# Performance work log

Measured on AMD Instinct MI355X. Metric: run time of the kernel, lower is better.

The kernel has to match this reference:

```python
import jax, jax.numpy as jnp
import numpy as np

N = 50000      # nodes
E = 800000     # edges (before self-loops)
D_IN = 64
D_OUT = 64


def setup_inputs() -> dict:
    key = jax.random.key(0)
    k1, k2, k3 = jax.random.split(key, 3)
    x = jax.random.normal(k1, (N, D_IN), dtype=jnp.float32)
    edge_index = jax.random.randint(k2, (2, E), 0, N, dtype=jnp.int64)
    # Glorot-ish init for the GCN linear weight
    W = jax.random.normal(k3, (D_IN, D_OUT), dtype=jnp.float32) * (1.0 / np.sqrt(D_IN))
    b = jnp.zeros((D_OUT,), dtype=jnp.float32)
    return {"x": x, "edge_index": edge_index, "W": W, "b": b}


def reference(x, edge_index, W, b):
    # GCNConv: add self-loops, symmetric normalization D^-1/2 (A+I) D^-1/2,
    # linear transform, scatter-add aggregation, bias; then ReLU.
    # Dropout is treated in eval mode (identity) for determinism.
    n = x.shape[0]
    loop = jnp.arange(n, dtype=edge_index.dtype)
    src = jnp.concatenate([edge_index[0], loop])  # [E+N]
    dst = jnp.concatenate([edge_index[1], loop])  # [E+N]

    ones = jnp.ones(src.shape[0], dtype=x.dtype)
    deg = jax.ops.segment_sum(ones, dst, num_segments=n)            # [N]
    dis = jnp.where(deg > 0, jax.lax.rsqrt(deg), 0.0)               # deg^-1/2
    norm = dis[src] * dis[dst]                                      # [E+N]

    xw = x @ W                                                      # [N, D_OUT]
    msgs = norm[:, None] * xw[src]                                  # [E+N, D_OUT]
    out = jax.ops.segment_sum(msgs, dst, num_segments=n) + b        # [N, D_OUT]
    return jax.nn.relu(out)
```

## Files before the change

### kernel.cpp

```cpp
#include <hip/hip_runtime.h>


#define TPB 256
#define STPB 512
#define MAXDEG 64
#define OVFCAP 8192
#define EPB 2048
#define MAXBIN 1024
#define MAXBLK 512

__device__ __forceinline__ int edges_are_i32(const unsigned* __restrict__ w) {
    int lane = threadIdx.x & 63;
    unsigned v = w[1 + 2 * lane];
    return __ballot(v != 0u) != 0ull;
}

__device__ __forceinline__ unsigned short f2bf(float f) {
    unsigned u = __float_as_uint(f);
    u += 0x7FFFu + ((u >> 16) & 1u);
    return (unsigned short)(u >> 16);
}
__device__ __forceinline__ float bf2f(unsigned short h) {
    return __uint_as_float(((unsigned)h) << 16);
}
__device__ __forceinline__ unsigned scale2(unsigned v, float dd) {
    unsigned lo = (unsigned)f2bf(dd * bf2f((unsigned short)(v & 0xFFFFu)));
    unsigned hi = (unsigned)f2bf(dd * bf2f((unsigned short)(v >> 16)));
    return lo | (hi << 16);
}

__device__ __forceinline__ void load4(const void* ei, int is32, long long base, int* v) {
    if (is32) {
        int4 a = *(const int4*)((const int*)ei + base);
        v[0] = a.x; v[1] = a.y; v[2] = a.z; v[3] = a.w;
    } else {
        longlong4 a = *(const longlong4*)((const long long*)ei + base);
        v[0] = (int)a.x; v[1] = (int)a.y; v[2] = (int)a.z; v[3] = (int)a.w;
    }
}

__global__ __launch_bounds__(512) void gemm_binsort(
        const float* __restrict__ x, const float* __restrict__ W,
        unsigned short* __restrict__ z0, unsigned* __restrict__ ovf,
        const void* __restrict__ ei, unsigned* __restrict__ arena,
        uint2* __restrict__ desc, int E, int nbins, int nblocks,
        int n, int gemmBlocks) {
    __shared__ __align__(16) unsigned char smem[22528];
    const int t = threadIdx.x;

    if ((int)blockIdx.x < gemmBlocks) {
        if (blockIdx.x == 0 && t == 0) *ovf = 0u;
        float* lw = (float*)smem;
#pragma unroll
        for (int i = 0; i < 8; ++i) lw[i * 512 + t] = W[i * 512 + t];
        __syncthreads();

        const int lane = t & 63;
        const int wv   = t >> 6;
        const int row0 = blockIdx.x * 64 + wv * 8;
        if (row0 >= n) return;
        const int nr = (n - row0 >= 8) ? 8 : (n - row0);

        float acc[8] = {0.f, 0.f, 0.f, 0.f, 0.f, 0.f, 0.f, 0.f};
#pragma unroll
        for (int k0 = 0; k0 < 16; ++k0) {
            const float w0 = lw[(4 * k0 + 0) * 64 + lane];
            const float w1 = lw[(4 * k0 + 1) * 64 + lane];
            const float w2 = lw[(4 * k0 + 2) * 64 + lane];
            const float w3 = lw[(4 * k0 + 3) * 64 + lane];
#pragma unroll
            for (int r = 0; r < 8; ++r) {
                if (r < nr) {
                    float4 xv = *(const float4*)(x + (long long)(row0 + r) * 64 + 4 * k0);
                    acc[r] = fmaf(xv.w, w3, fmaf(xv.z, w2, fmaf(xv.y, w1,
                             fmaf(xv.x, w0, acc[r]))));
                }
            }
        }
#pragma unroll
        for (int r = 0; r < 8; ++r)
            if (r < nr) z0[(long long)(row0 + r) * 64 + lane] = f2bf(acc[r]);
        return;
    }

    unsigned* hist    = (unsigned*)smem;
    unsigned* bstart  = hist + MAXBIN;
    unsigned* cur     = bstart + MAXBIN;
    unsigned* sorted  = cur + MAXBIN;
    unsigned* partial = sorted + EPB;
    const int blk = (int)blockIdx.x - gemmBlocks;
    const long long base = (long long)blk * EPB;
    const int cnt = (int)((E - base < EPB) ? (E - base) : EPB);
    const int is32 = edges_are_i32((const unsigned*)ei);

    for (int i = t; i < nbins; i += STPB) hist[i] = 0u;
    __syncthreads();

    unsigned pay[4];
    unsigned short bn[4];
    {
        const int lo = t * 4;
        if (lo + 4 <= cnt) {
            int s4[4], d4[4];
            load4(ei, is32, base + lo, s4);
            load4(ei, is32, (long long)E + base + lo, d4);
#pragma unroll
            for (int k = 0; k < 4; ++k) {
                pay[k] = ((unsigned)(d4[k] & 63) << 16) | (unsigned)s4[k];
                bn[k]  = (unsigned short)((unsigned)d4[k] >> 6);
                atomicAdd(&hist[bn[k]], 1u);
            }
        } else {
#pragma unroll
            for (int k = 0; k < 4; ++k) {
                int l = lo + k;
                if (l < cnt) {
                    int s_, d_;
                    if (is32) {
                        s_ = ((const int*)ei)[base + l];
                        d_ = ((const int*)ei)[(long long)E + base + l];
                    } else {
                        s_ = (int)((const long long*)ei)[base + l];
                        d_ = (int)((const long long*)ei)[(long long)E + base + l];
                    }
                    pay[k] = ((unsigned)(d_ & 63) << 16) | (unsigned)s_;
                    bn[k]  = (unsigned short)((unsigned)d_ >> 6);
                    atomicAdd(&hist[bn[k]], 1u);
                } else {
                    bn[k] = 0xFFFFu;
                }
            }
        }
    }
    __syncthreads();

    unsigned s0 = 0;
#pragma unroll
    for (int k = 0; k < 2; ++k) { int bq = t * 2 + k; if (bq < nbins) s0 += hist[bq]; }
    partial[t] = s0;
    __syncthreads();
    for (int o = 1; o < STPB; o <<= 1) {
        unsigned v = (t >= o) ? partial[t - o] : 0u;
        __syncthreads();
        partial[t] += v;
        __syncthreads();
    }
    unsigned run = (t == 0) ? 0u : partial[t - 1];
#pragma unroll
    for (int k = 0; k < 2; ++k) {
        int bq = t * 2 + k;
        if (bq < nbins) { bstart[bq] = run; cur[bq] = run; run += hist[bq]; }
    }
    __syncthreads();

#pragma unroll
    for (int i = 0; i < 4; ++i) {
        if (bn[i] != 0xFFFFu) {
            unsigned p = atomicAdd(&cur[bn[i]], 1u);
            sorted[p] = pay[i];
        }
    }
    __syncthreads();

    for (int i = t; i < cnt; i += STPB) arena[base + i] = sorted[i];
    for (int bq = t; bq < nbins; bq += STPB) {
        uint2 dd;
        dd.x = (unsigned)(base + bstart[bq]);
        dd.y = hist[bq];
        desc[(long long)blk * nbins + bq] = dd;
    }
}

__global__ __launch_bounds__(256) void build_ell(const uint2* __restrict__ desc,
                                                 const unsigned* __restrict__ arena,
                                                 unsigned* __restrict__ fc,
                                                 unsigned short* __restrict__ ell,
                                                 unsigned* __restrict__ ovf,
                                                 int* __restrict__ ovfList,
                                                 unsigned short* __restrict__ z,
                                                 int n, int nbins, int nblocks) {
    __shared__ unsigned segstart[MAXBLK];
    __shared__ unsigned segpre[MAXBLK];
    __shared__ unsigned pre[MAXBLK];
    __shared__ unsigned lcnt[MAXDEG];
    __shared__ __align__(16) unsigned short lell[MAXDEG * MAXDEG];
    const int t   = threadIdx.x;
    const int bin = blockIdx.x;
    const int base = bin * MAXDEG;

    if (t < MAXDEG) lcnt[t] = 0u;

    unsigned len0 = 0, len1 = 0;
    if (t < nblocks) {
        uint2 dd = desc[(long long)t * nbins + bin];
        segstart[t] = dd.x;
        len0 = dd.y;
    }
    if (t + 256 < nblocks) {
        uint2 dd = desc[(long long)(t + 256) * nbins + bin];
        segstart[t + 256] = dd.x;
        len1 = dd.y;
    }
    pre[t] = len0;
    pre[t + 256] = len1;
    __syncthreads();
    for (int o = 1; o < 256; o <<= 1) {
        unsigned vA = (t >= o) ? pre[t - o] : 0u;
        unsigned vB = (t >= o) ? pre[256 + t - o] : 0u;
        __syncthreads();
        pre[t] += vA;
        pre[256 + t] += vB;
        __syncthreads();
    }
    const unsigned lowTot = pre[255];
    pre[256 + t] += lowTot;
    __syncthreads();
    const unsigned total = pre[MAXBLK - 1];
    if (t < nblocks) segpre[t] = pre[t] - len0;
    if (t + 256 < nblocks) segpre[t + 256] = pre[256 + t] - len1;
    __syncthreads();

    for (unsigned j = t; j < total; j += 256) {
        int lo = 0, hi = nblocks - 1;
        while (lo < hi) {
            int mid = (lo + hi + 1) >> 1;
            if (segpre[mid] <= j) lo = mid; else hi = mid - 1;
        }
        unsigned e  = arena[segstart[lo] + (j - segpre[lo])];
        unsigned dl = e >> 16;
        unsigned c  = atomicAdd(&lcnt[dl], 1u);
        if (c < MAXDEG) {
            lell[dl * MAXDEG + c] = (unsigned short)(e & 0xFFFFu);
        } else {
            unsigned p = atomicAdd(ovf, 1u);
            if (p < OVFCAP) {
                ovfList[2 * p]     = (int)(e & 0xFFFFu);
                ovfList[2 * p + 1] = base + (int)dl;
            }
        }
    }
    __syncthreads();

    const int maxrow = (n - base < MAXDEG) ? (n - base) : MAXDEG;
    if (t < maxrow) fc[base + t] = lcnt[t];

    const uint4* lp = (const uint4*)lell;
    uint4* gp = (uint4*)(ell + (long long)base * MAXDEG);
    for (int i = t; i < maxrow * 8; i += 256) gp[i] = lp[i];

    uint4* zp = (uint4*)(z + (long long)base * 64);
    for (int i = t; i < maxrow * 8; i += 256) {
        int row = i >> 3;
        float dd = rsqrtf(1.0f + (float)lcnt[row]);
        uint4 v = zp[i];
        v.x = scale2(v.x, dd); v.y = scale2(v.y, dd);
        v.z = scale2(v.z, dd); v.w = scale2(v.w, dd);
        zp[i] = v;
    }
}

__global__ __launch_bounds__(256) void gather_z(const unsigned short* __restrict__ ell,
                                                const unsigned* __restrict__ fc,
                                                const unsigned* __restrict__ ovf,
                                                const int* __restrict__ ovfList,
                                                const unsigned short* __restrict__ z,
                                                const float* __restrict__ b,
                                                float* __restrict__ out, int n) {
    const int wv   = (int)threadIdx.x >> 6;
    const int lane = threadIdx.x & 63;
    const int half = lane >> 5;
    const int cp   = lane & 31;
    const int node = (blockIdx.x * 4 + wv) * 2 + half;
    const bool valid = node < n;
    const int nodec = valid ? node : (n - 1);

    const unsigned deg = valid ? fc[nodec] : 0u;
    const float dd = rsqrtf(1.0f + (float)deg);

    unsigned zs = *(const unsigned*)(z + (unsigned)nodec * 64 + cp * 2);
    float acc0 = bf2f((unsigned short)(zs & 0xFFFFu));
    float acc1 = bf2f((unsigned short)(zs >> 16));

    unsigned m = deg < MAXDEG ? deg : MAXDEG;
    if (!valid) m = 0u;
    const unsigned mo = __shfl_xor((int)m, 32);
    const unsigned mmax = m > mo ? m : mo;

    const uint4* prow = (const uint4*)(ell + (unsigned)nodec * MAXDEG);

    unsigned i = 0;
    for (; i + 8 <= mmax; i += 8) {
        uint4 rw = prow[i >> 3];
        unsigned s[8];
        s[0] = rw.x & 0xFFFFu; s[1] = rw.x >> 16;
        s[2] = rw.y & 0xFFFFu; s[3] = rw.y >> 16;
        s[4] = rw.z & 0xFFFFu; s[5] = rw.z >> 16;
        s[6] = rw.w & 0xFFFFu; s[7] = rw.w >> 16;
        if (i + 8 <= m) {
            unsigned v[8];
#pragma unroll
            for (int k = 0; k < 8; ++k)
                v[k] = *(const unsigned*)(z + s[k] * 64u + cp * 2);
#pragma unroll
            for (int k = 0; k < 8; ++k) {
                acc0 += bf2f((unsigned short)(v[k] & 0xFFFFu));
                acc1 += bf2f((unsigned short)(v[k] >> 16));
            }
        } else {
#pragma unroll
            for (int k = 0; k < 8; ++k) {
                if (i + k < m) {
                    unsigned v = *(const unsigned*)(z + s[k] * 64u + cp * 2);
                    acc0 += bf2f((unsigned short)(v & 0xFFFFu));
                    acc1 += bf2f((unsigned short)(v >> 16));
                }
            }
        }
    }
    for (; i < mmax; ++i) {
        if (i < m) {
            unsigned s = ell[(unsigned)nodec * MAXDEG + i];
            unsigned v = *(const unsigned*)(z + s * 64u + cp * 2);
            acc0 += bf2f((unsigned short)(v & 0xFFFFu));
            acc1 += bf2f((unsigned short)(v >> 16));
        }
    }

    unsigned nov = *ovf;
    if (nov > 0) {
        nov = nov < OVFCAP ? nov : OVFCAP;
        for (unsigned j = 0; j < nov; ++j)
            if (valid && ovfList[2 * j + 1] == node) {
                unsigned v = *(const unsigned*)(z + (unsigned)ovfList[2 * j] * 64u + cp * 2);
                acc0 += bf2f((unsigned short)(v & 0xFFFFu));
                acc1 += bf2f((unsigned short)(v >> 16));
            }
    }

    if (valid) {
        float2 o;
        o.x = fmaxf(fmaf(dd, acc0, b[cp * 2 + 0]), 0.f);
        o.y = fmaxf(fmaf(dd, acc1, b[cp * 2 + 1]), 0.f);
        *(float2*)(out + (unsigned)node * 64 + cp * 2) = o;
    }
}

extern "C" void kernel_launch(void* const* d_in, const int* in_sizes, int n_in,
                              void* d_out, int out_size, void* d_ws, size_t ws_size,
                              hipStream_t stream) {
    const float* x  = (const float*)d_in[0];
    const void*  ei = d_in[1];
    const float* W  = (const float*)d_in[2];
    const float* b  = (const float*)d_in[3];
    float* out = (float*)d_out;

    const int n = in_sizes[0] / 64;
    const int E = in_sizes[1] / 2;
    const int nbins   = (n + MAXDEG - 1) / MAXDEG;
    const int nblocks = (E + EPB - 1) / EPB;
    const int gemmBlocks = (n + 63) / 64;

    unsigned short* z       = (unsigned short*)d_ws;
    unsigned short* ell     = z + (long long)n * 64;
    unsigned*       fc      = (unsigned*)(ell + (long long)n * 64);
    unsigned*       ovf     = fc + n;
    int*            ovfList = (int*)(ovf + 1);
    unsigned*       arena   = (unsigned*)(ovfList + 2 * OVFCAP);
    uint2*          desc    = (uint2*)(arena + E);

    gemm_binsort<<<gemmBlocks + nblocks, STPB, 0, stream>>>(
        x, W, z, ovf, ei, arena, desc, E, nbins, nblocks, n, gemmBlocks);
    build_ell<<<nbins, TPB, 0, stream>>>(desc, arena, fc, ell, ovf, ovfList, z,
                                         n, nbins, nblocks);
    gather_z<<<(n + 7) / 8, TPB, 0, stream>>>(ell, fc, ovf, ovfList, z, b, out, n);
}
```

Measured before the change: 80.92 us.

## Widen gather to 16-byte loads per lane and add segment LUT in build_ell

The gather kernel is remapped so each lane handles 8 bf16 channels with uint4 loads and 8 nodes share a wavefront, instead of 2 channels per lane with 2 nodes per wave. This cuts the number of load instructions per neighbour row and lets the output be written with nontemporal float4 stores. In build_ell, a shared-memory lookup table maps edge positions to source segments, replacing the per-edge binary search for the first 2048 entries. The trade-offs are more registers per lane, more divergence when degrees differ across the 8 nodes in a wave, and the cost of filling the LUT serially per thread.

```diff
diff --git a/kernel.cpp b/kernel.cpp
--- a/kernel.cpp
+++ b/kernel.cpp
@@ -8,6 +8,9 @@
 #define EPB 2048
 #define MAXBIN 1024
 #define MAXBLK 512
+#define LUTSZ 2048
+
+typedef float fvec4 __attribute__((ext_vector_type(4)));
 
 __device__ __forceinline__ int edges_are_i32(const unsigned* __restrict__ w) {
     int lane = threadIdx.x & 63;
@@ -183,6 +186,7 @@
     __shared__ unsigned segpre[MAXBLK];
     __shared__ unsigned pre[MAXBLK];
     __shared__ unsigned lcnt[MAXDEG];
+    __shared__ unsigned short lut[LUTSZ];
     __shared__ __align__(16) unsigned short lell[MAXDEG * MAXDEG];
     const int t   = threadIdx.x;
     const int bin = blockIdx.x;
@@ -216,15 +220,28 @@
     pre[256 + t] += lowTot;
     __syncthreads();
     const unsigned total = pre[MAXBLK - 1];
-    if (t < nblocks) segpre[t] = pre[t] - len0;
-    if (t + 256 < nblocks) segpre[t + 256] = pre[256 + t] - len1;
+    unsigned sp0 = 0, sp1 = 0;
+    if (t < nblocks) { sp0 = pre[t] - len0; segpre[t] = sp0; }
+    if (t + 256 < nblocks) { sp1 = pre[256 + t] - len1; segpre[t + 256] = sp1; }
+    __syncthreads();
+
+    for (unsigned k = 0; k < len0 && sp0 + k < LUTSZ; ++k)
+        lut[sp0 + k] = (unsigned short)t;
+    for (unsigned k = 0; k < len1 && sp1 + k < LUTSZ; ++k)
+        lut[sp1 + k] = (unsigned short)(t + 256);
     __syncthreads();
 
     for (unsigned j = t; j < total; j += 256) {
-        int lo = 0, hi = nblocks - 1;
-        while (lo < hi) {
-            int mid = (lo + hi + 1) >> 1;
-            if (segpre[mid] <= j) lo = mid; else hi = mid - 1;
+        int lo;
+        if (j < LUTSZ) {
+            lo = (int)lut[j];
+        } else {
+            int l = 0, hi = nblocks - 1;
+            while (l < hi) {
+                int mid = (l + hi + 1) >> 1;
+                if (segpre[mid] <= j) l = mid; else hi = mid - 1;
+            }
+            lo = l;
         }
         unsigned e  = arena[segstart[lo] + (j - segpre[lo])];
         unsigned dl = e >> 16;
@@ -268,23 +285,34 @@
                                                 float* __restrict__ out, int n) {
     const int wv   = (int)threadIdx.x >> 6;
     const int lane = threadIdx.x & 63;
-    const int half = lane >> 5;
-    const int cp   = lane & 31;
-    const int node = (blockIdx.x * 4 + wv) * 2 + half;
+    const int o    = lane >> 3;
+    const int cp   = lane & 7;
+    const int node = (blockIdx.x * 4 + wv) * 8 + o;
     const bool valid = node < n;
     const int nodec = valid ? node : (n - 1);
 
     const unsigned deg = valid ? fc[nodec] : 0u;
     const float dd = rsqrtf(1.0f + (float)deg);
 
-    unsigned zs = *(const unsigned*)(z + (unsigned)nodec * 64 + cp * 2);
-    float acc0 = bf2f((unsigned short)(zs & 0xFFFFu));
-    float acc1 = bf2f((unsigned short)(zs >> 16));
+    uint4 zs = *(const uint4*)(z + (unsigned)nodec * 64 + cp * 8);
+    float a0 = bf2f((unsigned short)(zs.x & 0xFFFFu));
+    float a1 = bf2f((unsigned short)(zs.x >> 16));
+    float a2 = bf2f((unsigned short)(zs.y & 0xFFFFu));
+    float a3 = bf2f((unsigned short)(zs.y >> 16));
+    float a4 = bf2f((unsigned short)(zs.z & 0xFFFFu));
+    float a5 = bf2f((unsigned short)(zs.z >> 16));
+    float a6 = bf2f((unsigned short)(zs.w & 0xFFFFu));
+    float a7 = bf2f((unsigned short)(zs.w >> 16));
 
     unsigned m = deg < MAXDEG ? deg : MAXDEG;
     if (!valid) m = 0u;
-    const unsigned mo = __shfl_xor((int)m, 32);
-    const unsigned mmax = m > mo ? m : mo;
+    unsigned mm = m;
+    {
+        unsigned q1 = (unsigned)__shfl_xor((int)mm, 8);  mm = mm > q1 ? mm : q1;
+        unsigned q2 = (unsigned)__shfl_xor((int)mm, 16); mm = mm > q2 ? mm : q2;
+        unsigned q3 = (unsigned)__shfl_xor((int)mm, 32); mm = mm > q3 ? mm : q3;
+    }
+    const unsigned mmax = mm;
 
     const uint4* prow = (const uint4*)(ell + (unsigned)nodec * MAXDEG);
 
@@ -297,22 +325,34 @@
         s[4] = rw.z & 0xFFFFu; s[5] = rw.z >> 16;
         s[6] = rw.w & 0xFFFFu; s[7] = rw.w >> 16;
         if (i + 8 <= m) {
-            unsigned v[8];
+            uint4 v[8];
 #pragma unroll
             for (int k = 0; k < 8; ++k)
-                v[k] = *(const unsigned*)(z + s[k] * 64u + cp * 2);
+                v[k] = *(const uint4*)(z + s[k] * 64u + cp * 8);
 #pragma unroll
             for (int k = 0; k < 8; ++k) {
-                acc0 += bf2f((unsigned short)(v[k] & 0xFFFFu));
-                acc1 += bf2f((unsigned short)(v[k] >> 16));
+                a0 += bf2f((unsigned short)(v[k].x & 0xFFFFu));
+                a1 += bf2f((unsigned short)(v[k].x >> 16));
+                a2 += bf2f((unsigned short)(v[k].y & 0xFFFFu));
+                a3 += bf2f((unsigned short)(v[k].y >> 16));
+                a4 += bf2f((unsigned short)(v[k].z & 0xFFFFu));
+                a5 += bf2f((unsigned short)(v[k].z >> 16));
+                a6 += bf2f((unsigned short)(v[k].w & 0xFFFFu));
+                a7 += bf2f((unsigned short)(v[k].w >> 16));
             }
         } else {
 #pragma unroll
             for (int k = 0; k < 8; ++k) {
                 if (i + k < m) {
-                    unsigned v = *(const unsigned*)(z + s[k] * 64u + cp * 2);
-                    acc0 += bf2f((unsigned short)(v & 0xFFFFu));
-                    acc1 += bf2f((unsigned short)(v >> 16));
+                    uint4 v = *(const uint4*)(z + s[k] * 64u + cp * 8);
+                    a0 += bf2f((unsigned short)(v.x & 0xFFFFu));
+                    a1 += bf2f((unsigned short)(v.x >> 16));
+                    a2 += bf2f((unsigned short)(v.y & 0xFFFFu));
+                    a3 += bf2f((unsigned short)(v.y >> 16));
+                    a4 += bf2f((unsigned short)(v.z & 0xFFFFu));
+                    a5 += bf2f((unsigned short)(v.z >> 16));
+                    a6 += bf2f((unsigned short)(v.w & 0xFFFFu));
+                    a7 += bf2f((unsigned short)(v.w >> 16));
                 }
             }
         }
@@ -320,9 +360,15 @@
     for (; i < mmax; ++i) {
         if (i < m) {
             unsigned s = ell[(unsigned)nodec * MAXDEG + i];
-            unsigned v = *(const unsigned*)(z + s * 64u + cp * 2);
-            acc0 += bf2f((unsigned short)(v & 0xFFFFu));
-            acc1 += bf2f((unsigned short)(v >> 16));
+            uint4 v = *(const uint4*)(z + s * 64u + cp * 8);
+            a0 += bf2f((unsigned short)(v.x & 0xFFFFu));
+            a1 += bf2f((unsigned short)(v.x >> 16));
+            a2 += bf2f((unsigned short)(v.y & 0xFFFFu));
+            a3 += bf2f((unsigned short)(v.y >> 16));
+            a4 += bf2f((unsigned short)(v.z & 0xFFFFu));
+            a5 += bf2f((unsigned short)(v.z >> 16));
+            a6 += bf2f((unsigned short)(v.w & 0xFFFFu));
+            a7 += bf2f((unsigned short)(v.w >> 16));
         }
     }
 
@@ -331,17 +377,32 @@
         nov = nov < OVFCAP ? nov : OVFCAP;
         for (unsigned j = 0; j < nov; ++j)
             if (valid && ovfList[2 * j + 1] == node) {
-                unsigned v = *(const unsigned*)(z + (unsigned)ovfList[2 * j] * 64u + cp * 2);
-                acc0 += bf2f((unsigned short)(v & 0xFFFFu));
-                acc1 += bf2f((unsigned short)(v >> 16));
+                uint4 v = *(const uint4*)(z + (unsigned)ovfList[2 * j] * 64u + cp * 8);
+                a0 += bf2f((unsigned short)(v.x & 0xFFFFu));
+                a1 += bf2f((unsigned short)(v.x >> 16));
+                a2 += bf2f((unsigned short)(v.y & 0xFFFFu));
+                a3 += bf2f((unsigned short)(v.y >> 16));
+                a4 += bf2f((unsigned short)(v.z & 0xFFFFu));
+                a5 += bf2f((unsigned short)(v.z >> 16));
+                a6 += bf2f((unsigned short)(v.w & 0xFFFFu));
+                a7 += bf2f((unsigned short)(v.w >> 16));
             }
     }
 
     if (valid) {
-        float2 o;
-        o.x = fmaxf(fmaf(dd, acc0, b[cp * 2 + 0]), 0.f);
-        o.y = fmaxf(fmaf(dd, acc1, b[cp * 2 + 1]), 0.f);
-        *(float2*)(out + (unsigned)node * 64 + cp * 2) = o;
+        float4 b0 = *(const float4*)(b + cp * 8);
+        float4 b1 = *(const float4*)(b + cp * 8 + 4);
+        fvec4 o0, o1;
+        o0.x = fmaxf(fmaf(dd, a0, b0.x), 0.f);
+        o0.y = fmaxf(fmaf(dd, a1, b0.y), 0.f);
+        o0.z = fmaxf(fmaf(dd, a2, b0.z), 0.f);
+        o0.w = fmaxf(fmaf(dd, a3, b0.w), 0.f);
+        o1.x = fmaxf(fmaf(dd, a4, b1.x), 0.f);
+        o1.y = fmaxf(fmaf(dd, a5, b1.y), 0.f);
+        o1.z = fmaxf(fmaf(dd, a6, b1.z), 0.f);
+        o1.w = fmaxf(fmaf(dd, a7, b1.w), 0.f);
+        __builtin_nontemporal_store(o0, (fvec4*)(out + (unsigned)node * 64 + cp * 8));
+        __builtin_nontemporal_store(o1, (fvec4*)(out + (unsigned)node * 64 + cp * 8 + 4));
     }
 }
 
@@ -372,5 +433,5 @@
         x, W, z, ovf, ei, arena, desc, E, nbins, nblocks, n, gemmBlocks);
     build_ell<<<nbins, TPB, 0, stream>>>(desc, arena, fc, ell, ovf, ovfList, z,
                                          n, nbins, nblocks);
-    gather_z<<<(n + 7) / 8, TPB, 0, stream>>>(ell, fc, ovf, ovfList, z, b, out, n);
-}
+    gather_z<<<(n + 31) / 32, TPB, 0, stream>>>(ell, fc, ovf, ovfList, z, b, out, n);
+}
```

After: 76.06 us. -6.0%, faster.
